# Performance work log

Hardware: AMD Instinct MI355X
Metric: run time of the kernel (lower is better)

The kernel has to match this reference:

```python
import jax, jax.numpy as jnp
import numpy as np
from jax import lax

EPS = 1e-20
BN_EPS = 1e-5
ATTN_SCALE = 2.8284271247461903  # sqrt(d_l=8)
NS = (32, 32, 32, 10)
DS = (8, 8, 8, 16)


def squash(x):
    # Efficient-CapsNet squash: (1 - 1/(exp(||x||)+eps)) * x/(||x||+eps)
    norm = jnp.linalg.norm(x, axis=-1, keepdims=True)
    return (1.0 - 1.0 / (jnp.exp(norm) + EPS)) * (x / (norm + EPS))


def conv2d(x, w, b, stride, groups=1):
    y = lax.conv_general_dilated(
        x, w, window_strides=(stride, stride), padding='VALID',
        dimension_numbers=('NCHW', 'OIHW', 'NCHW'),
        feature_group_count=groups)
    return y + b[None, :, None, None]


def bn(x, g, b, m, v):
    inv = g / jnp.sqrt(v + BN_EPS)
    return x * inv[None, :, None, None] + (b - m * inv)[None, :, None, None]


def fccaps(U_l, W):
    # U_l: (b, n_l, d_l), W: (n_l, n_h, d_l, d_h)
    U_hat = jnp.einsum('bij,ikjl->bikl', U_l, W)          # (b, n_l, n_h, d_h)
    A = jnp.einsum('bikl,bhkl->bhik', U_hat, U_hat)        # (b, n_l, n_l, n_h)
    A_sum = jnp.sum(A, axis=-2)                            # (b, n_l, n_h)
    C = jax.nn.softmax(A_sum / ATTN_SCALE, axis=-1)        # (b, n_l, n_h)
    U_h = jnp.einsum('bikl,bik->bkl', U_hat, C)            # (b, n_h, d_h)
    return squash(U_h)


def setup_inputs() -> dict:
    key = jax.random.key(0)
    ks = jax.random.split(key, 8)
    B = 512
    x = jax.random.normal(ks[0], (B, 1, 39, 39), dtype=jnp.float32)
    conv1_w = jax.random.normal(ks[1], (128, 1, 3, 3), jnp.float32) * 0.2
    conv1_b = jnp.zeros((128,), jnp.float32)
    conv2_w = jax.random.normal(ks[2], (256, 128, 3, 3), jnp.float32) * 0.04
    conv2_b = jnp.zeros((256,), jnp.float32)
    conv3_w = jax.random.normal(ks[3], (256, 1, 9, 9), jnp.float32) * 0.1  # depthwise
    conv3_b = jnp.zeros((256,), jnp.float32)
    bn1_g = jnp.ones((128,), jnp.float32); bn1_b = jnp.zeros((128,), jnp.float32)
    bn1_m = jnp.zeros((128,), jnp.float32); bn1_v = jnp.ones((128,), jnp.float32)
    bn2_g = jnp.ones((256,), jnp.float32); bn2_b = jnp.zeros((256,), jnp.float32)
    bn2_m = jnp.zeros((256,), jnp.float32); bn2_v = jnp.ones((256,), jnp.float32)
    # capsule weights, kaiming-ish scale sqrt(2/fan_in) with fan_in = n_h*d_l*d_h
    def caps_w(k, n_l, n_h, d_l, d_h):
        std = np.sqrt(2.0 / (n_h * d_l * d_h))
        return jax.random.normal(k, (n_l, n_h, d_l, d_h), jnp.float32) * std
    W1 = caps_w(ks[4], NS[0], NS[1], DS[0], DS[1])
    W2 = caps_w(ks[5], NS[1], NS[2], DS[1], DS[2])
    W3 = caps_w(ks[6], NS[2], NS[3], DS[2], DS[3])
    return dict(x=x, conv1_w=conv1_w, conv1_b=conv1_b,
                bn1_g=bn1_g, bn1_b=bn1_b, bn1_m=bn1_m, bn1_v=bn1_v,
                conv2_w=conv2_w, conv2_b=conv2_b,
                bn2_g=bn2_g, bn2_b=bn2_b, bn2_m=bn2_m, bn2_v=bn2_v,
                conv3_w=conv3_w, conv3_b=conv3_b, W1=W1, W2=W2, W3=W3)


def reference(x, conv1_w, conv1_b, bn1_g, bn1_b, bn1_m, bn1_v,
              conv2_w, conv2_b, bn2_g, bn2_b, bn2_m, bn2_v,
              conv3_w, conv3_b, W1, W2, W3):
    h = jax.nn.relu(bn(conv2d(x, conv1_w, conv1_b, 2), bn1_g, bn1_b, bn1_m, bn1_v))
    h = jax.nn.relu(bn(conv2d(h, conv2_w, conv2_b, 2), bn2_g, bn2_b, bn2_m, bn2_v))
    h = conv2d(h, conv3_w, conv3_b, 1, groups=256)        # (B, 256, 1, 1)
    u = h.reshape(h.shape[0], NS[0], DS[0])                # (B, 32, 8)
    u = squash(u)
    for W in (W1, W2, W3):
        u = fccaps(u, W)
    return u  # (B, 10, 16)
```

## Files before the change

kernel.cpp:

```cpp
#include <hip/hip_runtime.h>


typedef __attribute__((ext_vector_type(8))) short short8;
typedef __attribute__((ext_vector_type(4))) float f32x4;

__device__ __forceinline__ ushort f2bf(float x) {
    uint u = __float_as_uint(x);
    return (ushort)((u + 0x7FFFu + ((u >> 16) & 1u)) >> 16);
}
__device__ __forceinline__ void bfsplit(float x, ushort& h, ushort& l) {
    h = f2bf(x);
    float hf = __uint_as_float(((uint)h) << 16);
    l = f2bf(x - hf);
}

__global__ __launch_bounds__(256) void k_prep(
    const float* __restrict__ w2, uint* __restrict__ Bt,
    const float* __restrict__ w3, float* __restrict__ w3T,
    const float* __restrict__ W1, const float* __restrict__ W2,
    const float* __restrict__ W3, float* __restrict__ Wr1,
    float* __restrict__ Wr2, float* __restrict__ Wr3,
    const float* __restrict__ c1b, const float* __restrict__ g1,
    const float* __restrict__ b1, const float* __restrict__ m1,
    const float* __restrict__ v1, float2* __restrict__ sc1) {
    __shared__ __align__(16) float wbuf[64 * 288];
    const int b = blockIdx.x, t = threadIdx.x;
    if (b < 144) {
        const int sidx = b >> 2, coq = b & 3;
        const int chunk = sidx / 9, tap = sidx - chunk * 9;
        const int co0 = coq * 64;
        for (int idx = t; idx < 4608; idx += 256) {
            const int n = idx / 72, q = idx - n * 72;
            ((float4*)wbuf)[n * 72 + q] =
                *(const float4*)(w2 + (size_t)(co0 + n) * 1152 + chunk * 288 + q * 4);
        }
        __syncthreads();
        const int n = t & 63, dg = (t >> 6) * 4;
        const int cot = coq >> 1, nn = ((coq & 1) * 64) + n;
        uint* dst = Bt + (size_t)(sidx * 2 + cot) * 4096;
#pragma unroll
        for (int dd = 0; dd < 4; ++dd) {
            const int d = dg + dd;
            const float x = wbuf[n * 288 + (2 * d) * 9 + tap];
            const float y = wbuf[n * 288 + (2 * d + 1) * 9 + tap];
            ushort xh, xl, yh, yl;
            bfsplit(x, xh, xl);
            bfsplit(y, yh, yl);
            dst[nn * 16 + d]        = (uint)xh | ((uint)yh << 16);
            dst[2048 + nn * 16 + d] = (uint)xl | ((uint)yl << 16);
        }
    } else if (b < 225) {
        const int p = b - 144;
        w3T[p * 256 + t] = w3[t * 81 + p];
    } else if (b < 321) {
        const int bb = b - 225;
        const int layer = bb >> 5, blk = bb & 31;
        const float* src = layer == 0 ? W1 : (layer == 1 ? W2 : W3);
        float* dst = layer == 0 ? Wr1 : (layer == 1 ? Wr2 : Wr3);
        const int d_h = (layer == 2) ? 16 : 8;
        const int total = (layer == 2) ? 5120 : 8192;
        for (int idx = blk * 256 + t; idx < 8 * total; idx += 32 * 256) {
            const int j = idx / total, e = idx - j * total;
            const int ik = e / d_h, l = e - ik * d_h;
            dst[idx] = src[(ik * 8 + j) * d_h + l];
        }
    } else {
        if (t < 128) {
            const float inv = g1[t] * rsqrtf(v1[t] + 1e-5f);
            sc1[t] = make_float2(inv, c1b[t] * inv + b1[t] - m1[t] * inv);
        }
    }
}

__global__ __launch_bounds__(256, 3) void k_conv2(
    const float* __restrict__ x, const float* __restrict__ w1,
    const float2* __restrict__ sc1, const uint* __restrict__ Bt,
    const float* __restrict__ g,
    const float* __restrict__ bb, const float* __restrict__ bm,
    const float* __restrict__ bv, const float* __restrict__ bias,
    const float* __restrict__ w3T, float* __restrict__ Uws) {
    __shared__ __align__(16) uint raw[11552];
    __shared__ __align__(16) float xs[1560];
    __shared__ float ured[128];
    const int t = threadIdx.x;
    const int lane = t & 63, wave = t >> 6;
    const int ln15 = lane & 15, lq = lane >> 4;
    const int wm = (wave >> 1) * 48, wn = (wave & 1) * 64;
    const int gg = blockIdx.x;
    const int bi  = ((gg >> 4) << 3) | (gg & 7);
    const int cot = (gg >> 3) & 1;
    const int co0 = cot * 128;

    const float* xb = x + (size_t)bi * 1521;
    for (int i = t; i < 1521; i += 256) {
        const int y = i / 39, xc = i - y * 39;
        xs[y * 40 + xc] = xb[i];
    }

    const int hc = t & 7, o2 = hc >> 1, half = hc & 1, pg = t >> 3;

    int PE[3], PO[3];
#pragma unroll
    for (int i = 0; i < 3; ++i) {
        const int m = wm + i * 16 + ln15;
        const int p = m < 81 ? m : 80;
        const int oh = p / 9, ow = p - oh * 9;
        PE[i] = lq * 760 + oh * 80 + ow * 4;
        PO[i] = 3040 + lq * 684 + oh * 72 + ow * 4;
    }
    int BRDg[4];
#pragma unroll
    for (int j = 0; j < 4; ++j) {
        const int n = wn + j * 16 + ln15;
        BRDg[j] = n * 16 + lq * 4;
    }

    f32x4 acc[3][4] = {};
    uint4 Bn[8];
    {
        const uint* bp = Bt + (size_t)cot * 4096;
#pragma unroll
        for (int j = 0; j < 4; ++j) {
            Bn[j]     = *(const uint4*)(bp + BRDg[j]);
            Bn[4 + j] = *(const uint4*)(bp + 2048 + BRDg[j]);
        }
    }

#pragma unroll
    for (int c = 0; c < 4; ++c) {
        const int o = c * 4 + o2;
        float wr[36];
        {
            const float4* wp = reinterpret_cast<const float4*>(w1 + o * 72 + half * 36);
#pragma unroll
            for (int q = 0; q < 9; ++q) {
                const float4 wv = wp[q];
                wr[q * 4 + 0] = wv.x; wr[q * 4 + 1] = wv.y;
                wr[q * 4 + 2] = wv.z; wr[q * 4 + 3] = wv.w;
            }
        }
        float2 ssv[4];
#pragma unroll
        for (int jj = 0; jj < 4; ++jj) ssv[jj] = sc1[o * 8 + half * 4 + jj];

        __syncthreads();

        {
            ushort* rawu = (ushort*)raw;
            for (int p = pg; p < 361; p += 32) {
                const int y = p / 19, xq = p - y * 19;
                const int b2 = y * 80 + xq * 2;
                const float2 x01 = *(const float2*)(xs + b2);
                const float  x2v = xs[b2 + 2];
                const float2 x34 = *(const float2*)(xs + b2 + 40);
                const float  x5v = xs[b2 + 42];
                const float2 x67 = *(const float2*)(xs + b2 + 80);
                const float  x8v = xs[b2 + 82];
                uint hw0, hw1, lw0, lw1;
                {
                    uint hv[4], lv[4];
#pragma unroll
                    for (int jj = 0; jj < 4; ++jj) {
                        const float a = x01.x * wr[jj * 9 + 0] + x01.y * wr[jj * 9 + 1] +
                                        x2v   * wr[jj * 9 + 2] + x34.x * wr[jj * 9 + 3] +
                                        x34.y * wr[jj * 9 + 4] + x5v   * wr[jj * 9 + 5] +
                                        x67.x * wr[jj * 9 + 6] + x67.y * wr[jj * 9 + 7] +
                                        x8v   * wr[jj * 9 + 8];
                        const float v = fmaxf(fmaf(a, ssv[jj].x, ssv[jj].y), 0.0f);
                        const uint u = __float_as_uint(v);
                        hv[jj] = u >> 16;
                        const float d = v - __uint_as_float(u & 0xFFFF0000u);
                        lv[jj] = __float_as_uint(d) >> 16;
                    }
                    hw0 = hv[0] | (hv[1] << 16);
                    hw1 = hv[2] | (hv[3] << 16);
                    lw0 = lv[0] | (lv[1] << 16);
                    lw1 = lv[2] | (lv[3] << 16);
                }
                int ad;
                if ((xq & 1) == 0) {
                    ad = o2 * 1520 + (y * 10 + (xq >> 1)) * 8 + half * 4;
                } else {
                    ad = 6080 + o2 * 1368 + (y * 9 + (xq >> 1)) * 8 + half * 4;
                }
                *(uint2*)(rawu + ad)         = make_uint2(hw0, hw1);
                *(uint2*)(rawu + 11552 + ad) = make_uint2(lw0, lw1);
            }
        }
        __syncthreads();

        short8 a_h[3];
#pragma unroll
        for (int i = 0; i < 3; ++i)
            a_h[i] = *reinterpret_cast<const short8*>(raw + PE[i]);
#pragma unroll
        for (int tap = 0; tap < 9; ++tap) {
            const int s = c * 9 + tap;
            uint4 Bc[8];
#pragma unroll
            for (int q = 0; q < 8; ++q) Bc[q] = Bn[q];
            if (s < 35) {
                const uint* bp = Bt + (size_t)((s + 1) * 2 + cot) * 4096;
#pragma unroll
                for (int j = 0; j < 4; ++j) {
                    Bn[j]     = *(const uint4*)(bp + BRDg[j]);
                    Bn[4 + j] = *(const uint4*)(bp + 2048 + BRDg[j]);
                }
            }
            const int kh = tap / 3, kw = tap - kh * 3;
            const int odd = kw & 1;
            const int sE = kh * 40 + (kw >> 1) * 4;
            const int sO = kh * 36;
            short8 a_l[3];
#pragma unroll
            for (int i = 0; i < 3; ++i) {
                const int addr = odd ? (PO[i] + sO) : (PE[i] + sE);
                a_l[i] = *reinterpret_cast<const short8*>(raw + addr + 5776);
            }
            short8 a_hn[3];
            if (tap < 8) {
                const int tap2 = tap + 1;
                const int kh2 = tap2 / 3, kw2 = tap2 - kh2 * 3;
                const int odd2 = kw2 & 1;
                const int sE2 = kh2 * 40 + (kw2 >> 1) * 4;
                const int sO2 = kh2 * 36;
#pragma unroll
                for (int i = 0; i < 3; ++i) {
                    const int addr2 = odd2 ? (PO[i] + sO2) : (PE[i] + sE2);
                    a_hn[i] = *reinterpret_cast<const short8*>(raw + addr2);
                }
            }
            short8 bh[4], bl[4];
#pragma unroll
            for (int j = 0; j < 4; ++j) {
                bh[j] = __builtin_bit_cast(short8, Bc[j]);
                bl[j] = __builtin_bit_cast(short8, Bc[4 + j]);
            }
#pragma unroll
            for (int i = 0; i < 3; ++i)
#pragma unroll
                for (int j = 0; j < 4; ++j)
                    acc[i][j] = __builtin_amdgcn_mfma_f32_16x16x32_bf16(a_h[i], bh[j], acc[i][j], 0, 0, 0);
#pragma unroll
            for (int i = 0; i < 3; ++i)
#pragma unroll
                for (int j = 0; j < 4; ++j)
                    acc[i][j] = __builtin_amdgcn_mfma_f32_16x16x32_bf16(a_h[i], bl[j], acc[i][j], 0, 0, 0);
#pragma unroll
            for (int i = 0; i < 3; ++i)
#pragma unroll
                for (int j = 0; j < 4; ++j)
                    acc[i][j] = __builtin_amdgcn_mfma_f32_16x16x32_bf16(a_l[i], bh[j], acc[i][j], 0, 0, 0);
            if (tap < 8) {
#pragma unroll
                for (int i = 0; i < 3; ++i) a_h[i] = a_hn[i];
            }
        }
    }

    float scj[4], shj[4];
#pragma unroll
    for (int j = 0; j < 4; ++j) {
        const int co = co0 + wn + j * 16 + ln15;
        const float inv = g[co] * rsqrtf(bv[co] + 1e-5f);
        scj[j] = inv;
        shj[j] = bias[co] * inv + bb[co] - bm[co] * inv;
    }
    float usum[4] = {0.f, 0.f, 0.f, 0.f};
#pragma unroll
    for (int i = 0; i < 3; ++i)
#pragma unroll
        for (int r = 0; r < 4; ++r) {
            const int m = wm + i * 16 + lq * 4 + r;
            if (m < 81) {
                const float* wrow = w3T + m * 256 + co0;
#pragma unroll
                for (int j = 0; j < 4; ++j) {
                    const int col = wn + j * 16 + ln15;
                    const float v = fmaxf(fmaf(acc[i][j][r], scj[j], shj[j]), 0.0f);
                    usum[j] = fmaf(v, wrow[col], usum[j]);
                }
            }
        }
#pragma unroll
    for (int j = 0; j < 4; ++j) {
        usum[j] += __shfl_xor(usum[j], 16);
        usum[j] += __shfl_xor(usum[j], 32);
    }
    if (lq == 0 && wm == 0) {
#pragma unroll
        for (int j = 0; j < 4; ++j) ured[(wn >> 6) * 64 + j * 16 + ln15] = usum[j];
    }
    __syncthreads();
    if (lq == 0 && wm == 48) {
#pragma unroll
        for (int j = 0; j < 4; ++j) {
            const int col = wn + j * 16 + ln15;
            Uws[(size_t)bi * 256 + co0 + col] =
                usum[j] + ured[(wn >> 6) * 64 + j * 16 + ln15];
        }
    }
}

__device__ __forceinline__ void fccaps_block(
    const int n_l, const int n_h, const int d_h, const float* __restrict__ Wr,
    float* U, float* Uh, float* Sv, float* Av, float* Cv, float* coefs,
    float* outU, const int t) {
    const int nkd = n_h * d_h;
    const int total = n_l * nkd;
    __syncthreads();
    for (int e = t; e < total; e += 256) {
        const int i = e / nkd;
        const float* up = U + i * 8;
        float acc = 0.0f;
#pragma unroll
        for (int j = 0; j < 8; ++j) acc += up[j] * Wr[j * total + e];
        Uh[e] = acc;
    }
    __syncthreads();
    for (int e = t; e < nkd; e += 256) {
        float acc = 0.0f;
        for (int i = 0; i < n_l; ++i) acc += Uh[i * nkd + e];
        Sv[e] = acc;
    }
    __syncthreads();
    for (int e = t; e < n_l * n_h; e += 256) {
        const int h = e / n_h, k = e - h * n_h;
        float acc = 0.0f;
        for (int l = 0; l < d_h; ++l)
            acc += Uh[h * nkd + k * d_h + l] * Sv[k * d_h + l];
        Av[e] = acc;
    }
    __syncthreads();
    {
        const int h = t >> 3, sub = t & 7;
        const float invs = 1.0f / 2.8284271247461903f;
        float mx = -1e30f;
        for (int k = sub; k < n_h; k += 8) mx = fmaxf(mx, Av[h * n_h + k]);
        mx = fmaxf(mx, __shfl_xor(mx, 1));
        mx = fmaxf(mx, __shfl_xor(mx, 2));
        mx = fmaxf(mx, __shfl_xor(mx, 4));
        float sum = 0.0f;
        for (int k = sub; k < n_h; k += 8) {
            const float ev = expf((Av[h * n_h + k] - mx) * invs);
            Cv[h * n_h + k] = ev;
            sum += ev;
        }
        sum += __shfl_xor(sum, 1);
        sum += __shfl_xor(sum, 2);
        sum += __shfl_xor(sum, 4);
        const float r = 1.0f / sum;
        for (int k = sub; k < n_h; k += 8) Cv[h * n_h + k] *= r;
    }
    __syncthreads();
    for (int e = t; e < nkd; e += 256) {
        const int k = e / d_h;
        float acc = 0.0f;
        for (int i = 0; i < n_l; ++i) acc += Uh[i * nkd + e] * Cv[i * n_h + k];
        Sv[e] = acc;
    }
    __syncthreads();
    if (t < n_h) {
        float ssq = 0.0f;
        for (int l = 0; l < d_h; ++l) { const float uv = Sv[t * d_h + l]; ssq += uv * uv; }
        const float n = sqrtf(ssq);
        coefs[t] = (1.0f - 1.0f / (expf(n) + 1e-20f)) / (n + 1e-20f);
    }
    __syncthreads();
    for (int e = t; e < nkd; e += 256) outU[e] = Sv[e] * coefs[e / d_h];
}

__global__ __launch_bounds__(256) void k_caps(
    const float* __restrict__ Uws, const float* __restrict__ b3,
    const float* __restrict__ Wr1, const float* __restrict__ Wr2,
    const float* __restrict__ Wr3, float* __restrict__ out) {
    __shared__ float U[256];
    __shared__ float Uh[8192];
    __shared__ float Sv[256];
    __shared__ float Av[1024];
    __shared__ float Cv[1024];
    __shared__ float coefs[32];
    const int b = blockIdx.x, t = threadIdx.x;
    U[t] = Uws[(size_t)b * 256 + t] + b3[t];
    __syncthreads();
    if (t < 32) {
        float ssq = 0.0f;
        for (int j = 0; j < 8; ++j) { const float uv = U[t * 8 + j]; ssq += uv * uv; }
        const float n = sqrtf(ssq);
        coefs[t] = (1.0f - 1.0f / (expf(n) + 1e-20f)) / (n + 1e-20f);
    }
    __syncthreads();
    U[t] *= coefs[t >> 3];
    fccaps_block(32, 32,  8, Wr1, U, Uh, Sv, Av, Cv, coefs, U, t);
    fccaps_block(32, 32,  8, Wr2, U, Uh, Sv, Av, Cv, coefs, U, t);
    fccaps_block(32, 10, 16, Wr3, U, Uh, Sv, Av, Cv, coefs, out + (size_t)b * 160, t);
}

extern "C" void kernel_launch(void* const* d_in, const int* in_sizes, int n_in,
                              void* d_out, int out_size, void* d_ws, size_t ws_size,
                              hipStream_t stream) {
    const float* x    = (const float*)d_in[0];
    const float* c1w  = (const float*)d_in[1];
    const float* c1b  = (const float*)d_in[2];
    const float* bn1g = (const float*)d_in[3];
    const float* bn1b = (const float*)d_in[4];
    const float* bn1m = (const float*)d_in[5];
    const float* bn1v = (const float*)d_in[6];
    const float* c2w  = (const float*)d_in[7];
    const float* c2b  = (const float*)d_in[8];
    const float* bn2g = (const float*)d_in[9];
    const float* bn2b = (const float*)d_in[10];
    const float* bn2m = (const float*)d_in[11];
    const float* bn2v = (const float*)d_in[12];
    const float* c3w  = (const float*)d_in[13];
    const float* c3b  = (const float*)d_in[14];
    const float* W1   = (const float*)d_in[15];
    const float* W2   = (const float*)d_in[16];
    const float* W3   = (const float*)d_in[17];
    float* out = (float*)d_out;
    uint*  wsu = (uint*)d_ws;
    float* wsf = (float*)d_ws;

    float*  Uws = wsf;
    uint*   Bt  = wsu + 131072;
    float*  w3T = wsf + 425984;
    float*  Wr1 = wsf + 446720;
    float*  Wr2 = wsf + 512256;
    float*  Wr3 = wsf + 577792;
    float2* sc1 = (float2*)(wsf + 618752);

    k_prep<<<dim3(322), 256, 0, stream>>>(c2w, Bt, c3w, w3T, W1, W2, W3,
                                          Wr1, Wr2, Wr3,
                                          c1b, bn1g, bn1b, bn1m, bn1v, sc1);
    k_conv2<<<dim3(1024), 256, 0, stream>>>(x, c1w, sc1, Bt,
                                            bn2g, bn2b, bn2m, bn2v,
                                            c2b, w3T, Uws);
    k_caps<<<dim3(512), 256, 0, stream>>>(Uws, c3b, Wr1, Wr2, Wr3, out);
}
```

Baseline: 217.8 us.

## Merge both output-channel tiles into one 512-thread block per image

Launches one 512-thread block per image instead of two 256-thread blocks that each covered half of the conv2 output channels. The conv1+BN+ReLU staging into shared memory is therefore computed once per image rather than twice, with each thread now producing 2 channels instead of 4. Each wave picks its B tile from its own wave index. The launch bound changes to (512, 4), which may squeeze the register budget and cause spills, and fewer, larger blocks change how work is spread across the CUs.

Measured after the change: 204.9 us. 1.06x faster.

```diff
diff --git a/kernel.cpp b/kernel.cpp
--- a/kernel.cpp
+++ b/kernel.cpp
@@ -72,7 +72,7 @@
     }
 }
 
-__global__ __launch_bounds__(256, 3) void k_conv2(
+__global__ __launch_bounds__(512, 4) void k_conv2(
     const float* __restrict__ x, const float* __restrict__ w1,
     const float2* __restrict__ sc1, const uint* __restrict__ Bt,
     const float* __restrict__ g,
@@ -81,23 +81,22 @@
     const float* __restrict__ w3T, float* __restrict__ Uws) {
     __shared__ __align__(16) uint raw[11552];
     __shared__ __align__(16) float xs[1560];
-    __shared__ float ured[128];
+    __shared__ float ured[256];
     const int t = threadIdx.x;
     const int lane = t & 63, wave = t >> 6;
     const int ln15 = lane & 15, lq = lane >> 4;
-    const int wm = (wave >> 1) * 48, wn = (wave & 1) * 64;
-    const int gg = blockIdx.x;
-    const int bi  = ((gg >> 4) << 3) | (gg & 7);
-    const int cot = (gg >> 3) & 1;
-    const int co0 = cot * 128;
+    const int wm = (wave >> 2) * 48;
+    const int wn = (wave & 3) * 64;
+    const int cot_w = (wave & 3) >> 1;
+    const int bi = blockIdx.x;
 
     const float* xb = x + (size_t)bi * 1521;
-    for (int i = t; i < 1521; i += 256) {
+    for (int i = t; i < 1521; i += 512) {
         const int y = i / 39, xc = i - y * 39;
         xs[y * 40 + xc] = xb[i];
     }
 
-    const int hc = t & 7, o2 = hc >> 1, half = hc & 1, pg = t >> 3;
+    const int qc = t & 15, ol = qc >> 2, qo = (qc & 3) * 2, pg = t >> 4;
 
     int PE[3], PO[3];
 #pragma unroll
@@ -111,14 +110,14 @@
     int BRDg[4];
 #pragma unroll
     for (int j = 0; j < 4; ++j) {
-        const int n = wn + j * 16 + ln15;
+        const int n = ((wn & 64) + j * 16 + ln15);
         BRDg[j] = n * 16 + lq * 4;
     }
 
     f32x4 acc[3][4] = {};
     uint4 Bn[8];
     {
-        const uint* bp = Bt + (size_t)cot * 4096;
+        const uint* bp = Bt + (size_t)cot_w * 4096;
 #pragma unroll
         for (int j = 0; j < 4; ++j) {
             Bn[j]     = *(const uint4*)(bp + BRDg[j]);
@@ -128,20 +127,19 @@
 
 #pragma unroll
     for (int c = 0; c < 4; ++c) {
-        const int o = c * 4 + o2;
-        float wr[36];
+        const int o_g = c * 32 + qc * 2;
+        float wr[18];
         {
-            const float4* wp = reinterpret_cast<const float4*>(w1 + o * 72 + half * 36);
+            const float2* wp = reinterpret_cast<const float2*>(w1 + o_g * 9);
 #pragma unroll
             for (int q = 0; q < 9; ++q) {
-                const float4 wv = wp[q];
-                wr[q * 4 + 0] = wv.x; wr[q * 4 + 1] = wv.y;
-                wr[q * 4 + 2] = wv.z; wr[q * 4 + 3] = wv.w;
-            }
-        }
-        float2 ssv[4];
-#pragma unroll
-        for (int jj = 0; jj < 4; ++jj) ssv[jj] = sc1[o * 8 + half * 4 + jj];
+                const float2 wv = wp[q];
+                wr[q * 2] = wv.x; wr[q * 2 + 1] = wv.y;
+            }
+        }
+        float2 ssv[2];
+        ssv[0] = sc1[o_g];
+        ssv[1] = sc1[o_g + 1];
 
         __syncthreads();
 
@@ -156,11 +154,11 @@
                 const float  x5v = xs[b2 + 42];
                 const float2 x67 = *(const float2*)(xs + b2 + 80);
                 const float  x8v = xs[b2 + 82];
-                uint hw0, hw1, lw0, lw1;
+                uint hw, lw;
                 {
-                    uint hv[4], lv[4];
-#pragma unroll
-                    for (int jj = 0; jj < 4; ++jj) {
+                    uint hv[2], lv[2];
+#pragma unroll
+                    for (int jj = 0; jj < 2; ++jj) {
                         const float a = x01.x * wr[jj * 9 + 0] + x01.y * wr[jj * 9 + 1] +
                                         x2v   * wr[jj * 9 + 2] + x34.x * wr[jj * 9 + 3] +
                                         x34.y * wr[jj * 9 + 4] + x5v   * wr[jj * 9 + 5] +
@@ -172,19 +170,17 @@
                         const float d = v - __uint_as_float(u & 0xFFFF0000u);
                         lv[jj] = __float_as_uint(d) >> 16;
                     }
-                    hw0 = hv[0] | (hv[1] << 16);
-                    hw1 = hv[2] | (hv[3] << 16);
-                    lw0 = lv[0] | (lv[1] << 16);
-                    lw1 = lv[2] | (lv[3] << 16);
+                    hw = hv[0] | (hv[1] << 16);
+                    lw = lv[0] | (lv[1] << 16);
                 }
                 int ad;
                 if ((xq & 1) == 0) {
-                    ad = o2 * 1520 + (y * 10 + (xq >> 1)) * 8 + half * 4;
+                    ad = ol * 1520 + (y * 10 + (xq >> 1)) * 8 + qo;
                 } else {
-                    ad = 6080 + o2 * 1368 + (y * 9 + (xq >> 1)) * 8 + half * 4;
+                    ad = 6080 + ol * 1368 + (y * 9 + (xq >> 1)) * 8 + qo;
                 }
-                *(uint2*)(rawu + ad)         = make_uint2(hw0, hw1);
-                *(uint2*)(rawu + 11552 + ad) = make_uint2(lw0, lw1);
+                *(uint*)(rawu + ad)         = hw;
+                *(uint*)(rawu + 11552 + ad) = lw;
             }
         }
         __syncthreads();
@@ -200,7 +196,7 @@
 #pragma unroll
             for (int q = 0; q < 8; ++q) Bc[q] = Bn[q];
             if (s < 35) {
-                const uint* bp = Bt + (size_t)((s + 1) * 2 + cot) * 4096;
+                const uint* bp = Bt + (size_t)((s + 1) * 2 + cot_w) * 4096;
 #pragma unroll
                 for (int j = 0; j < 4; ++j) {
                     Bn[j]     = *(const uint4*)(bp + BRDg[j]);
@@ -261,7 +257,7 @@
     float scj[4], shj[4];
 #pragma unroll
     for (int j = 0; j < 4; ++j) {
-        const int co = co0 + wn + j * 16 + ln15;
+        const int co = wn + j * 16 + ln15;
         const float inv = g[co] * rsqrtf(bv[co] + 1e-5f);
         scj[j] = inv;
         shj[j] = bias[co] * inv + bb[co] - bm[co] * inv;
@@ -273,7 +269,7 @@
         for (int r = 0; r < 4; ++r) {
             const int m = wm + i * 16 + lq * 4 + r;
             if (m < 81) {
-                const float* wrow = w3T + m * 256 + co0;
+                const float* wrow = w3T + m * 256;
 #pragma unroll
                 for (int j = 0; j < 4; ++j) {
                     const int col = wn + j * 16 + ln15;
@@ -289,15 +285,14 @@
     }
     if (lq == 0 && wm == 0) {
 #pragma unroll
-        for (int j = 0; j < 4; ++j) ured[(wn >> 6) * 64 + j * 16 + ln15] = usum[j];
+        for (int j = 0; j < 4; ++j) ured[wn + j * 16 + ln15] = usum[j];
     }
     __syncthreads();
     if (lq == 0 && wm == 48) {
 #pragma unroll
         for (int j = 0; j < 4; ++j) {
             const int col = wn + j * 16 + ln15;
-            Uws[(size_t)bi * 256 + co0 + col] =
-                usum[j] + ured[(wn >> 6) * 64 + j * 16 + ln15];
+            Uws[(size_t)bi * 256 + col] = usum[j] + ured[col];
         }
     }
 }
@@ -432,8 +427,8 @@
     k_prep<<<dim3(322), 256, 0, stream>>>(c2w, Bt, c3w, w3T, W1, W2, W3,
                                           Wr1, Wr2, Wr3,
                                           c1b, bn1g, bn1b, bn1m, bn1v, sc1);
-    k_conv2<<<dim3(1024), 256, 0, stream>>>(x, c1w, sc1, Bt,
-                                            bn2g, bn2b, bn2m, bn2v,
-                                            c2b, w3T, Uws);
+    k_conv2<<<dim3(512), 512, 0, stream>>>(x, c1w, sc1, Bt,
+                                           bn2g, bn2b, bn2m, bn2v,
+                                           c2b, w3T, Uws);
     k_caps<<<dim3(512), 256, 0, stream>>>(Uws, c3b, Wr1, Wr2, Wr3, out);
 }
```
